# Performance work log

Hardware: AMD Instinct MI355X
Metric: run time of the kernel (lower is better)

## Reference

```python
import jax, jax.numpy as jnp
import numpy as np

E = 32      # particle_embed_dim = q/k/v head out dim
G = 2       # nof_net_types (conv groups)
NEG_SLOPE = 0.01


def _glin(x, w, b, groups):
    """Grouped 1x1 conv on (M, C, 1, 1) == grouped linear.
    x: (M, Cin), w: (Cout, Cin//groups), b: (Cout,)."""
    M = x.shape[0]
    Cout = w.shape[0]
    xg = x.reshape(M, groups, -1)                 # (M, G, Cin/G)
    wg = w.reshape(groups, Cout // groups, -1)    # (G, Cout/G, Cin/G)
    y = jnp.einsum('mgi,goi->mgo', xg, wg).reshape(M, Cout)
    return y + b


def setup_inputs() -> dict:
    key = jax.random.key(0)
    ks = jax.random.split(key, 9)
    B, N = 32, 1024
    s = 0.05
    return {
        'x_e':   jax.random.normal(ks[0], (B, N, G * E), dtype=jnp.float32),
        'w_qkv': jax.random.normal(ks[1], (3 * G * E, E), dtype=jnp.float32) * s,
        'b_qkv': jax.random.normal(ks[2], (3 * G * E,), dtype=jnp.float32) * s,
        'w_h1':  jax.random.normal(ks[3], (G * E, 2 * E), dtype=jnp.float32) * s,
        'b_h1':  jax.random.normal(ks[4], (G * E,), dtype=jnp.float32) * s,
        'w_h10': jax.random.normal(ks[5], (G * E, E), dtype=jnp.float32) * s,
        'b_h10': jax.random.normal(ks[6], (G * E,), dtype=jnp.float32) * s,
        'w_h11': jax.random.normal(ks[7], (G * E, E), dtype=jnp.float32) * s,
        'b_h11': jax.random.normal(ks[8], (G * E,), dtype=jnp.float32) * s,
    }


def reference(x_e, w_qkv, b_qkv, w_h1, b_h1, w_h10, b_h10, w_h11, b_h11):
    B, N, D = x_e.shape                      # D = G*E = 64
    act = lambda z: jnp.where(z >= 0, z, NEG_SLOPE * z)

    # grouped 1x1-conv QKV projection
    qkv = _glin(x_e.reshape(B * N, D), w_qkv, b_qkv, G)        # (B*N, 3*G*E)
    qkv = qkv.reshape(B, N, G, 3, E).transpose(0, 2, 3, 1, 4)  # (B, G, 3, N, E)
    q, k, v = qkv[:, :, 0], qkv[:, :, 1], qkv[:, :, 2]         # each (B, G, N, E)

    # NOTE: module divides k by sqrt(E) and logits by sqrt(E) again -> 1/E total
    scale = 1.0 / E
    ip = jnp.einsum('bgne,bgme->bgnm', q, k) * scale           # (B, G, N, N)
    sip = jax.nn.softmax(ip, axis=-1)
    attn = jnp.einsum('bgnm,bgme->bgne', sip, v)               # (B, G, N, E)

    # concat pre-attention v with attention output, regroup per-particle
    x_xe = jnp.concatenate([v, attn], axis=3)                  # (B, G, N, 2E)
    x_xe = x_xe.transpose(0, 2, 1, 3).reshape(B * N, G * 2 * E)  # (B*N, 128)

    h = act(_glin(x_xe, w_h1, b_h1, G))
    h = act(_glin(h, w_h10, b_h10, G))
    h = act(_glin(h, w_h11, b_h11, G))
    return h.reshape(B * N, G * E, 1, 1)
```

## Files before the change

### kernel.cpp

```cpp
#include <hip/hip_runtime.h>

#define B_ 32
#define N_ 1024
#define NEG 0.01f
#define QSC (1.4426950408889634f/32.0f)

using half8  = __attribute__((ext_vector_type(8))) _Float16;
using half4  = __attribute__((ext_vector_type(4))) _Float16;
using half2  = __attribute__((ext_vector_type(2))) _Float16;
using fp16x2 = __attribute__((ext_vector_type(2))) __fp16;
using floatx4 = __attribute__((ext_vector_type(4))) float;

#if defined(__has_builtin)
#if __has_builtin(__builtin_amdgcn_exp2f)
#define EXP2(x) __builtin_amdgcn_exp2f(x)
#endif
#endif
#ifndef EXP2
#define EXP2(x) exp2f(x)
#endif

__device__ inline half2 pkcvt(float a, float b) {
    fp16x2 r = __builtin_amdgcn_cvt_pkrtz(a, b);
    return __builtin_bit_cast(half2, r);
}

__device__ inline half8 cvt8(float4 a, float4 b) {
    half2 p0 = pkcvt(a.x, a.y);
    half2 p1 = pkcvt(a.z, a.w);
    half2 p2 = pkcvt(b.x, b.y);
    half2 p3 = pkcvt(b.z, b.w);
    half8 h = { p0[0],p0[1], p1[0],p1[1], p2[0],p2[1], p3[0],p3[1] };
    return h;
}

struct __align__(16) Smem {
    _Float16 wsh[96*36];
    float    bsh[96];
    _Float16 Kst[2][128*40];
    _Float16 Vtst[2][32*136];
    union {
        _Float16 qs[128*40];
        _Float16 xs[128*72];
    } u;
    float linv[128];
    float bl1[32], bl10[32], bl11[32];
};

__global__ __launch_bounds__(256, 2) void fused_kernel(
    const float* __restrict__ x, const float* __restrict__ w_qkv, const float* __restrict__ b_qkv,
    const float* __restrict__ w_h1,  const float* __restrict__ b_h1,
    const float* __restrict__ w_h10, const float* __restrict__ b_h10,
    const float* __restrict__ w_h11, const float* __restrict__ b_h11,
    float* __restrict__ out)
{
    __shared__ Smem sm;
    int t = threadIdx.x;
    int bg = blockIdx.x >> 3;
    int qtile = blockIdx.x & 7;
    int b = bg >> 1, g = bg & 1;
    int qbase = qtile * 128;
    int lane = t & 63, w = t >> 6;
    int L15 = lane & 15, quad = lane >> 4;

    for (int idx = t; idx < 96*32; idx += 256) {
        int r = idx >> 5, c = idx & 31;
        float wv = w_qkv[(g*96 + r)*32 + c];
        sm.wsh[r*36 + c] = (_Float16)(r < 32 ? wv*QSC : wv);
    }
    if (t < 96) sm.bsh[t] = b_qkv[g*96 + t];
    if (t < 32) {
        sm.bl1[t]  = b_h1[g*32+t];
        sm.bl10[t] = b_h10[g*32+t];
        sm.bl11[t] = b_h11[g*32+t];
    }
    __syncthreads();

    half8 bwq[2], bwk[2], bwv[2];
    floatx4 cq[2], ck[2], cv[2];
    #pragma unroll
    for (int et = 0; et < 2; et++) {
        bwq[et] = *(const half8*)&sm.wsh[(     et*16 + L15)*36 + quad*8];
        bwk[et] = *(const half8*)&sm.wsh[(32 + et*16 + L15)*36 + quad*8];
        bwv[et] = *(const half8*)&sm.wsh[(64 + et*16 + L15)*36 + quad*8];
        float bq = sm.bsh[     et*16 + L15] * QSC;
        float bk = sm.bsh[32 + et*16 + L15];
        float bv = sm.bsh[64 + et*16 + L15];
        cq[et] = (floatx4){bq,bq,bq,bq};
        ck[et] = (floatx4){bk,bk,bk,bk};
        cv[et] = (floatx4){bv,bv,bv,bv};
    }

    {
        floatx4 dq[2][2];
        #pragma unroll
        for (int mt = 0; mt < 2; mt++) {
            const float* p = x + ((size_t)b*N_ + qbase + w*32 + mt*16 + L15)*64 + g*32 + quad*8;
            half8 axq = cvt8(*(const float4*)p, *(const float4*)(p + 4));
            dq[mt][0] = __builtin_amdgcn_mfma_f32_16x16x32_f16(axq, bwq[0], cq[0], 0,0,0);
            dq[mt][1] = __builtin_amdgcn_mfma_f32_16x16x32_f16(axq, bwq[1], cq[1], 0,0,0);
        }
        #pragma unroll
        for (int mt = 0; mt < 2; mt++)
            #pragma unroll
            for (int et = 0; et < 2; et++)
                #pragma unroll
                for (int r = 0; r < 4; r++)
                    sm.u.qs[(w*32 + mt*16 + quad*4 + r)*40 + et*16 + L15] =
                        (_Float16)dq[mt][et][r];
    }
    __syncthreads();
    half8 bq0 = *(const half8*)&sm.u.qs[(w*32 +      L15)*40 + quad*8];
    half8 bq1 = *(const half8*)&sm.u.qs[(w*32 + 16 + L15)*40 + quad*8];

    float4 xf0[2], xf1[2];
    auto prefetch = [&](int tile) {
        #pragma unroll
        for (int mt = 0; mt < 2; mt++) {
            const float* p = x + ((size_t)b*N_ + tile*128 + w*32 + mt*16 + L15)*64 + g*32 + quad*8;
            xf0[mt] = *(const float4*)p;
            xf1[mt] = *(const float4*)(p + 4);
        }
    };
    auto proj_tile = [&](int tile, int buf) {
        floatx4 dK[2][2], dV[2][2];
        #pragma unroll
        for (int mt = 0; mt < 2; mt++) {
            half8 axk = cvt8(xf0[mt], xf1[mt]);
            dK[mt][0] = __builtin_amdgcn_mfma_f32_16x16x32_f16(axk, bwk[0], ck[0], 0,0,0);
            dK[mt][1] = __builtin_amdgcn_mfma_f32_16x16x32_f16(axk, bwk[1], ck[1], 0,0,0);
            dV[mt][0] = __builtin_amdgcn_mfma_f32_16x16x32_f16(axk, bwv[0], cv[0], 0,0,0);
            dV[mt][1] = __builtin_amdgcn_mfma_f32_16x16x32_f16(axk, bwv[1], cv[1], 0,0,0);
        }
        #pragma unroll
        for (int mt = 0; mt < 2; mt++) {
            int rb = w*32 + mt*16 + quad*4;
            #pragma unroll
            for (int et = 0; et < 2; et++) {
                half2 k01 = pkcvt(dK[mt][et][0], dK[mt][et][1]);
                half2 k23 = pkcvt(dK[mt][et][2], dK[mt][et][3]);
                half2 v01 = pkcvt(dV[mt][et][0], dV[mt][et][1]);
                half2 v23 = pkcvt(dV[mt][et][2], dV[mt][et][3]);
                half4 vh = { v01[0], v01[1], v23[0], v23[1] };
                sm.Kst[buf][(rb+0)*40 + et*16 + L15] = k01[0];
                sm.Kst[buf][(rb+1)*40 + et*16 + L15] = k01[1];
                sm.Kst[buf][(rb+2)*40 + et*16 + L15] = k23[0];
                sm.Kst[buf][(rb+3)*40 + et*16 + L15] = k23[1];
                *(half4*)&sm.Vtst[buf][(et*16 + L15)*136 + rb] = vh;
                if (tile == qtile) {
                    #pragma unroll
                    for (int r = 0; r < 4; r++)
                        sm.u.xs[(rb + r)*72 + et*16 + L15] = vh[r];
                }
            }
        }
    };

    prefetch(0);
    proj_tile(0, 0);
    __syncthreads();

    floatx4 o00 = {0.f,0.f,0.f,0.f}, o01 = o00, o10 = o00, o11 = o00;
    float lsum0 = 0.f, lsum1 = 0.f;

    for (int kt = 0; kt < 8; kt++) {
        int cur = kt & 1;
        if (kt < 7) prefetch(kt + 1);
        #pragma unroll
        for (int mt8 = 0; mt8 < 8; mt8++) {
            half8 ak = *(const half8*)&sm.Kst[cur][(mt8*16 + L15)*40 + quad*8];
            floatx4 zz = {0.f,0.f,0.f,0.f};
            floatx4 s0 = __builtin_amdgcn_mfma_f32_16x16x32_f16(ak, bq0, zz, 0,0,0);
            floatx4 s1 = __builtin_amdgcn_mfma_f32_16x16x32_f16(ak, bq1, zz, 0,0,0);
            float p00 = EXP2(s0.x), p01 = EXP2(s0.y), p02 = EXP2(s0.z), p03 = EXP2(s0.w);
            float p10 = EXP2(s1.x), p11 = EXP2(s1.y), p12 = EXP2(s1.z), p13 = EXP2(s1.w);
            lsum0 += (p00+p01)+(p02+p03);
            lsum1 += (p10+p11)+(p12+p13);
            half2 pa = pkcvt(p00, p01);
            half2 pb = pkcvt(p02, p03);
            half2 pc = pkcvt(p10, p11);
            half2 pd = pkcvt(p12, p13);
            half4 a0 = { pa[0], pa[1], pb[0], pb[1] };
            half4 a1 = { pc[0], pc[1], pd[0], pd[1] };
            half4 bv0 = *(const half4*)&sm.Vtst[cur][      L15*136 + mt8*16 + quad*4];
            half4 bv1 = *(const half4*)&sm.Vtst[cur][(16 + L15)*136 + mt8*16 + quad*4];
            o00 = __builtin_amdgcn_mfma_f32_16x16x16f16(a0, bv0, o00, 0,0,0);
            o01 = __builtin_amdgcn_mfma_f32_16x16x16f16(a0, bv1, o01, 0,0,0);
            o10 = __builtin_amdgcn_mfma_f32_16x16x16f16(a1, bv0, o10, 0,0,0);
            o11 = __builtin_amdgcn_mfma_f32_16x16x16f16(a1, bv1, o11, 0,0,0);
        }
        if (kt < 7) proj_tile(kt + 1, 1 - cur);
        __syncthreads();
    }

    lsum0 += __shfl_xor(lsum0, 16, 64); lsum0 += __shfl_xor(lsum0, 32, 64);
    lsum1 += __shfl_xor(lsum1, 16, 64); lsum1 += __shfl_xor(lsum1, 32, 64);
    if (quad == 0) {
        sm.linv[w*32 +      L15] = 1.0f / lsum0;
        sm.linv[w*32 + 16 + L15] = 1.0f / lsum1;
    }
    __syncthreads();

    {
        const floatx4* ofr[2][2] = { {&o00,&o01}, {&o10,&o11} };
        #pragma unroll
        for (int nt = 0; nt < 2; nt++) {
            float4 li = *(const float4*)&sm.linv[w*32 + nt*16 + quad*4];
            #pragma unroll
            for (int et = 0; et < 2; et++) {
                floatx4 ov = *ofr[nt][et];
                sm.u.xs[(w*32+nt*16+quad*4+0)*72 + 32 + et*16 + L15] = (_Float16)(ov[0]*li.x);
                sm.u.xs[(w*32+nt*16+quad*4+1)*72 + 32 + et*16 + L15] = (_Float16)(ov[1]*li.y);
                sm.u.xs[(w*32+nt*16+quad*4+2)*72 + 32 + et*16 + L15] = (_Float16)(ov[2]*li.z);
                sm.u.xs[(w*32+nt*16+quad*4+3)*72 + 32 + et*16 + L15] = (_Float16)(ov[3]*li.w);
            }
        }
    }
    __syncthreads();

    half4 a1f[2][4], a2f[2][2], a3f[2][2];
    #pragma unroll
    for (int mt = 0; mt < 2; mt++) {
        #pragma unroll
        for (int kt = 0; kt < 4; kt++) {
            float4 f = *(const float4*)(w_h1 + (size_t)(g*32+mt*16+L15)*64 + kt*16 + quad*4);
            half2 ha = pkcvt(f.x, f.y);
            half2 hb = pkcvt(f.z, f.w);
            half4 h = { ha[0], ha[1], hb[0], hb[1] };
            a1f[mt][kt] = h;
        }
        #pragma unroll
        for (int kt = 0; kt < 2; kt++) {
            float4 f = *(const float4*)(w_h10 + (size_t)(g*32+mt*16+L15)*32 + kt*16 + quad*4);
            half2 ha = pkcvt(f.x, f.y);
            half2 hb = pkcvt(f.z, f.w);
            half4 h = { ha[0], ha[1], hb[0], hb[1] };
            a2f[mt][kt] = h;
            float4 f2 = *(const float4*)(w_h11 + (size_t)(g*32+mt*16+L15)*32 + kt*16 + quad*4);
            half2 hc = pkcvt(f2.x, f2.y);
            half2 hd = pkcvt(f2.z, f2.w);
            half4 h2 = { hc[0], hc[1], hd[0], hd[1] };
            a3f[mt][kt] = h2;
        }
    }

    floatx4 d1[2][2];
    #pragma unroll
    for (int mt = 0; mt < 2; mt++) {
        float4 bb = *(const float4*)&sm.bl1[mt*16 + quad*4];
        floatx4 seed = { bb.x, bb.y, bb.z, bb.w };
        d1[mt][0] = seed; d1[mt][1] = seed;
    }
    #pragma unroll
    for (int nt = 0; nt < 2; nt++)
        #pragma unroll
        for (int kt = 0; kt < 4; kt++) {
            half4 b1 = *(const half4*)&sm.u.xs[(w*32+nt*16+L15)*72 + kt*16 + quad*4];
            d1[0][nt] = __builtin_amdgcn_mfma_f32_16x16x16f16(a1f[0][kt], b1, d1[0][nt], 0,0,0);
            d1[1][nt] = __builtin_amdgcn_mfma_f32_16x16x16f16(a1f[1][kt], b1, d1[1][nt], 0,0,0);
        }
    half4 h1b[2][2];
    #pragma unroll
    for (int mt = 0; mt < 2; mt++)
        #pragma unroll
        for (int nt = 0; nt < 2; nt++) {
            float v0 = d1[mt][nt][0]; v0 = (v0>=0.f)?v0:NEG*v0;
            float v1 = d1[mt][nt][1]; v1 = (v1>=0.f)?v1:NEG*v1;
            float v2 = d1[mt][nt][2]; v2 = (v2>=0.f)?v2:NEG*v2;
            float v3 = d1[mt][nt][3]; v3 = (v3>=0.f)?v3:NEG*v3;
            half2 ha = pkcvt(v0, v1);
            half2 hb = pkcvt(v2, v3);
            half4 h = { ha[0], ha[1], hb[0], hb[1] };
            h1b[mt][nt] = h;
        }
    floatx4 d2[2][2];
    #pragma unroll
    for (int mt = 0; mt < 2; mt++) {
        float4 bb = *(const float4*)&sm.bl10[mt*16 + quad*4];
        floatx4 seed = { bb.x, bb.y, bb.z, bb.w };
        d2[mt][0] = seed; d2[mt][1] = seed;
    }
    #pragma unroll
    for (int mt = 0; mt < 2; mt++)
        #pragma unroll
        for (int nt = 0; nt < 2; nt++)
            #pragma unroll
            for (int kt = 0; kt < 2; kt++)
                d2[mt][nt] = __builtin_amdgcn_mfma_f32_16x16x16f16(a2f[mt][kt], h1b[kt][nt], d2[mt][nt], 0,0,0);
    half4 h2b[2][2];
    #pragma unroll
    for (int mt = 0; mt < 2; mt++)
        #pragma unroll
        for (int nt = 0; nt < 2; nt++) {
            float v0 = d2[mt][nt][0]; v0 = (v0>=0.f)?v0:NEG*v0;
            float v1 = d2[mt][nt][1]; v1 = (v1>=0.f)?v1:NEG*v1;
            float v2 = d2[mt][nt][2]; v2 = (v2>=0.f)?v2:NEG*v2;
            float v3 = d2[mt][nt][3]; v3 = (v3>=0.f)?v3:NEG*v3;
            half2 ha = pkcvt(v0, v1);
            half2 hb = pkcvt(v2, v3);
            half4 h = { ha[0], ha[1], hb[0], hb[1] };
            h2b[mt][nt] = h;
        }
    floatx4 d3[2][2];
    #pragma unroll
    for (int mt = 0; mt < 2; mt++) {
        float4 bb = *(const float4*)&sm.bl11[mt*16 + quad*4];
        floatx4 seed = { bb.x, bb.y, bb.z, bb.w };
        d3[mt][0] = seed; d3[mt][1] = seed;
    }
    #pragma unroll
    for (int mt = 0; mt < 2; mt++)
        #pragma unroll
        for (int nt = 0; nt < 2; nt++)
            #pragma unroll
            for (int kt = 0; kt < 2; kt++)
                d3[mt][nt] = __builtin_amdgcn_mfma_f32_16x16x16f16(a3f[mt][kt], h2b[kt][nt], d3[mt][nt], 0,0,0);
    #pragma unroll
    for (int mt = 0; mt < 2; mt++)
        #pragma unroll
        for (int nt = 0; nt < 2; nt++) {
            float4 ov;
            ov.x = d3[mt][nt][0]; ov.x = (ov.x>=0.f)?ov.x:NEG*ov.x;
            ov.y = d3[mt][nt][1]; ov.y = (ov.y>=0.f)?ov.y:NEG*ov.y;
            ov.z = d3[mt][nt][2]; ov.z = (ov.z>=0.f)?ov.z:NEG*ov.z;
            ov.w = d3[mt][nt][3]; ov.w = (ov.w>=0.f)?ov.w:NEG*ov.w;
            *(float4*)(out + ((size_t)b*N_ + qbase + w*32 + nt*16 + L15)*64 + g*32 + mt*16 + quad*4) = ov;
        }
}

extern "C" void kernel_launch(void* const* d_in, const int* in_sizes, int n_in,
                              void* d_out, int out_size, void* d_ws, size_t ws_size,
                              hipStream_t stream) {
    const float* x_e   = (const float*)d_in[0];
    const float* w_qkv = (const float*)d_in[1];
    const float* b_qkv = (const float*)d_in[2];
    const float* w_h1  = (const float*)d_in[3];
    const float* b_h1  = (const float*)d_in[4];
    const float* w_h10 = (const float*)d_in[5];
    const float* b_h10 = (const float*)d_in[6];
    const float* w_h11 = (const float*)d_in[7];
    const float* b_h11 = (const float*)d_in[8];
    float* out = (float*)d_out;

    hipLaunchKernelGGL(fused_kernel, dim3(B_*2*8), dim3(256), 0, stream,
                       x_e, w_qkv, b_qkv, w_h1, b_h1, w_h10, b_h10, w_h11, b_h11, out);
}
```

Measured before the change: 98.32 us.

## Split QKV projection into separate kernel and stream fp16 K/V via LDS DMA

The single fused kernel, which recomputed the K/V projection for every key tile in every query block, becomes two kernels. A projection kernel writes Q, K, V and transposed V in fp16 to workspace once. The attention kernel then streams K/V tiles straight into LDS with global_load_lds double buffering and uses a swizzled V layout. It runs smaller 64-query blocks with two waves splitting the key range, merging partial sums through LDS, raises occupancy to 4 blocks per SM and remaps block indices. This removes the redundant projection work, at the cost of an extra launch and a global-memory round trip through the workspace.

```diff
diff --git a/kernel.cpp b/kernel.cpp
--- a/kernel.cpp
+++ b/kernel.cpp
@@ -20,6 +20,9 @@
 #define EXP2(x) exp2f(x)
 #endif
 
+#define MFMA32 __builtin_amdgcn_mfma_f32_16x16x32_f16
+#define MFMA16 __builtin_amdgcn_mfma_f32_16x16x16f16
+
 __device__ inline half2 pkcvt(float a, float b) {
     fp16x2 r = __builtin_amdgcn_cvt_pkrtz(a, b);
     return __builtin_bit_cast(half2, r);
@@ -34,32 +37,33 @@
     return h;
 }
 
-struct __align__(16) Smem {
-    _Float16 wsh[96*36];
-    float    bsh[96];
-    _Float16 Kst[2][128*40];
-    _Float16 Vtst[2][32*136];
-    union {
-        _Float16 qs[128*40];
-        _Float16 xs[128*72];
-    } u;
-    float linv[128];
-    float bl1[32], bl10[32], bl11[32];
-};
-
-__global__ __launch_bounds__(256, 2) void fused_kernel(
+__device__ __forceinline__ void gload16(const _Float16* g, _Float16* l) {
+#if defined(__has_builtin) && __has_builtin(__builtin_amdgcn_global_load_lds)
+    __builtin_amdgcn_global_load_lds(
+        (const __attribute__((address_space(1))) unsigned int*)g,
+        (__attribute__((address_space(3))) unsigned int*)l, 16, 0, 0);
+#else
+    int lane = threadIdx.x & 63;
+    *(half8*)(l + lane*8) = *(const half8*)g;
+#endif
+}
+
+__global__ __launch_bounds__(256, 2) void proj_kernel(
     const float* __restrict__ x, const float* __restrict__ w_qkv, const float* __restrict__ b_qkv,
-    const float* __restrict__ w_h1,  const float* __restrict__ b_h1,
-    const float* __restrict__ w_h10, const float* __restrict__ b_h10,
-    const float* __restrict__ w_h11, const float* __restrict__ b_h11,
-    float* __restrict__ out)
+    _Float16* __restrict__ Qs, _Float16* __restrict__ Kg,
+    _Float16* __restrict__ Vg, _Float16* __restrict__ Vtg)
 {
-    __shared__ Smem sm;
+    __shared__ struct __align__(16) {
+        _Float16 wsh[96*36];
+        float    bsh[96];
+        _Float16 qk[128*72];
+        _Float16 vrow[128*32];
+        _Float16 vt[32*136];
+    } sm;
     int t = threadIdx.x;
     int bg = blockIdx.x >> 3;
-    int qtile = blockIdx.x & 7;
+    int qt = blockIdx.x & 7;
     int b = bg >> 1, g = bg & 1;
-    int qbase = qtile * 128;
     int lane = t & 63, w = t >> 6;
     int L15 = lane & 15, quad = lane >> 4;
 
@@ -69,11 +73,6 @@
         sm.wsh[r*36 + c] = (_Float16)(r < 32 ? wv*QSC : wv);
     }
     if (t < 96) sm.bsh[t] = b_qkv[g*96 + t];
-    if (t < 32) {
-        sm.bl1[t]  = b_h1[g*32+t];
-        sm.bl10[t] = b_h10[g*32+t];
-        sm.bl11[t] = b_h11[g*32+t];
-    }
     __syncthreads();
 
     half8 bwq[2], bwk[2], bwv[2];
@@ -91,87 +90,126 @@
         cv[et] = (floatx4){bv,bv,bv,bv};
     }
 
+    #pragma unroll
+    for (int mt = 0; mt < 2; mt++) {
+        const float* p = x + ((size_t)b*N_ + qt*128 + w*32 + mt*16 + L15)*64 + g*32 + quad*8;
+        half8 ax = cvt8(*(const float4*)p, *(const float4*)(p + 4));
+        floatx4 dQ[2], dK[2], dV[2];
+        #pragma unroll
+        for (int et = 0; et < 2; et++) {
+            dQ[et] = MFMA32(ax, bwq[et], cq[et], 0,0,0);
+            dK[et] = MFMA32(ax, bwk[et], ck[et], 0,0,0);
+            dV[et] = MFMA32(ax, bwv[et], cv[et], 0,0,0);
+        }
+        int rb = w*32 + mt*16 + quad*4;
+        #pragma unroll
+        for (int et = 0; et < 2; et++) {
+            #pragma unroll
+            for (int r = 0; r < 4; r++)
+                sm.qk[(rb+r)*72 + et*16 + L15] = (_Float16)dQ[et][r];
+            half2 k01 = pkcvt(dK[et][0], dK[et][1]);
+            half2 k23 = pkcvt(dK[et][2], dK[et][3]);
+            sm.qk[(rb+0)*72 + 32 + et*16 + L15] = k01[0];
+            sm.qk[(rb+1)*72 + 32 + et*16 + L15] = k01[1];
+            sm.qk[(rb+2)*72 + 32 + et*16 + L15] = k23[0];
+            sm.qk[(rb+3)*72 + 32 + et*16 + L15] = k23[1];
+            half2 v01 = pkcvt(dV[et][0], dV[et][1]);
+            half2 v23 = pkcvt(dV[et][2], dV[et][3]);
+            half4 vh = { v01[0], v01[1], v23[0], v23[1] };
+            sm.vrow[(rb+0)*32 + et*16 + L15] = vh[0];
+            sm.vrow[(rb+1)*32 + et*16 + L15] = vh[1];
+            sm.vrow[(rb+2)*32 + et*16 + L15] = vh[2];
+            sm.vrow[(rb+3)*32 + et*16 + L15] = vh[3];
+            *(half4*)&sm.vt[(et*16 + L15)*136 + rb] = vh;
+        }
+    }
+    __syncthreads();
+
     {
-        floatx4 dq[2][2];
-        #pragma unroll
-        for (int mt = 0; mt < 2; mt++) {
-            const float* p = x + ((size_t)b*N_ + qbase + w*32 + mt*16 + L15)*64 + g*32 + quad*8;
-            half8 axq = cvt8(*(const float4*)p, *(const float4*)(p + 4));
-            dq[mt][0] = __builtin_amdgcn_mfma_f32_16x16x32_f16(axq, bwq[0], cq[0], 0,0,0);
-            dq[mt][1] = __builtin_amdgcn_mfma_f32_16x16x32_f16(axq, bwq[1], cq[1], 0,0,0);
-        }
-        #pragma unroll
-        for (int mt = 0; mt < 2; mt++)
-            #pragma unroll
-            for (int et = 0; et < 2; et++)
-                #pragma unroll
-                for (int r = 0; r < 4; r++)
-                    sm.u.qs[(w*32 + mt*16 + quad*4 + r)*40 + et*16 + L15] =
-                        (_Float16)dq[mt][et][r];
-    }
-    __syncthreads();
-    half8 bq0 = *(const half8*)&sm.u.qs[(w*32 +      L15)*40 + quad*8];
-    half8 bq1 = *(const half8*)&sm.u.qs[(w*32 + 16 + L15)*40 + quad*8];
-
-    float4 xf0[2], xf1[2];
-    auto prefetch = [&](int tile) {
-        #pragma unroll
-        for (int mt = 0; mt < 2; mt++) {
-            const float* p = x + ((size_t)b*N_ + tile*128 + w*32 + mt*16 + L15)*64 + g*32 + quad*8;
-            xf0[mt] = *(const float4*)p;
-            xf1[mt] = *(const float4*)(p + 4);
+        int row = t >> 1, sel = t & 1;
+        const float4* s4 = (const float4*)&sm.qk[row*72 + sel*32];
+        float4* d4 = (float4*)((sel ? Kg : Qs) + ((size_t)bg*1024 + qt*128 + row)*32);
+        d4[0]=s4[0]; d4[1]=s4[1]; d4[2]=s4[2]; d4[3]=s4[3];
+    }
+    if (t < 128) {
+        const float4* s4 = (const float4*)&sm.vrow[t*32];
+        float4* d4 = (float4*)(Vg + ((size_t)bg*1024 + qt*128 + t)*32);
+        d4[0]=s4[0]; d4[1]=s4[1]; d4[2]=s4[2]; d4[3]=s4[3];
+    }
+    {
+        int e = t >> 3, c = t & 7;
+        const float4* s4 = (const float4*)&sm.vt[e*136 + c*16];
+        float4* d4 = (float4*)(Vtg + ((size_t)bg*32 + e)*1024 + qt*128 + c*16);
+        d4[0]=s4[0]; d4[1]=s4[1];
+    }
+}
+
+__global__ __launch_bounds__(256, 4) void attn_kernel(
+    const _Float16* __restrict__ Qs, const _Float16* __restrict__ Kg,
+    const _Float16* __restrict__ Vg, const _Float16* __restrict__ Vtg,
+    const float* __restrict__ w_h1,  const float* __restrict__ b_h1,
+    const float* __restrict__ w_h10, const float* __restrict__ b_h10,
+    const float* __restrict__ w_h11, const float* __restrict__ b_h11,
+    float* __restrict__ out)
+{
+    __shared__ struct __align__(16) {
+        _Float16 Kt[2][2][64*32];
+        _Float16 Vt[2][2][32*64];
+        _Float16 xs[64*40];
+        float    linv[64];
+    } sm;
+    int t = threadIdx.x;
+    int bid = blockIdx.x;
+    int map = (bid & 7)*128 + (bid >> 3);
+    int bg = map >> 4, qt = map & 15;
+    int b = bg >> 1, g = bg & 1;
+    int lane = t & 63, w = t >> 6;
+    int L15 = lane & 15, quad = lane >> 4;
+    int qg = w >> 1, h = w & 1;
+    int qbase = qt*64;
+    int lr = qg*32;
+    int l7s = (L15 & 7) << 3;
+
+    const _Float16* qrow = Qs + ((size_t)bg*1024 + qbase + lr)*32;
+    half8 bq0 = *(const half8*)(qrow + (size_t)L15*32 + quad*8);
+    half8 bq1 = *(const half8*)(qrow + (size_t)(16 + L15)*32 + quad*8);
+
+    const _Float16* kg0 = Kg + (size_t)bg*32768 + lane*8;
+    int er = lane >> 3;
+    int vswz = ((lane & 7)*8) ^ (er << 3);
+    const _Float16* vg0 = Vtg + (size_t)bg*32768 + (size_t)er*1024 + vswz;
+
+    auto stage = [&](int tile, int buf) {
+        _Float16* kl = &sm.Kt[buf][h][0];
+        _Float16* vl = &sm.Vt[buf][h][0];
+        const _Float16* kgt = kg0 + (size_t)tile*2048;
+        const _Float16* vgt = vg0 + (size_t)tile*64;
+        #pragma unroll
+        for (int c = 0; c < 2; c++) {
+            int cc = qg*2 + c;
+            gload16(kgt + cc*512,          kl + cc*512);
+            gload16(vgt + (size_t)cc*8192, vl + cc*512);
         }
     };
-    auto proj_tile = [&](int tile, int buf) {
-        floatx4 dK[2][2], dV[2][2];
-        #pragma unroll
-        for (int mt = 0; mt < 2; mt++) {
-            half8 axk = cvt8(xf0[mt], xf1[mt]);
-            dK[mt][0] = __builtin_amdgcn_mfma_f32_16x16x32_f16(axk, bwk[0], ck[0], 0,0,0);
-            dK[mt][1] = __builtin_amdgcn_mfma_f32_16x16x32_f16(axk, bwk[1], ck[1], 0,0,0);
-            dV[mt][0] = __builtin_amdgcn_mfma_f32_16x16x32_f16(axk, bwv[0], cv[0], 0,0,0);
-            dV[mt][1] = __builtin_amdgcn_mfma_f32_16x16x32_f16(axk, bwv[1], cv[1], 0,0,0);
-        }
-        #pragma unroll
-        for (int mt = 0; mt < 2; mt++) {
-            int rb = w*32 + mt*16 + quad*4;
-            #pragma unroll
-            for (int et = 0; et < 2; et++) {
-                half2 k01 = pkcvt(dK[mt][et][0], dK[mt][et][1]);
-                half2 k23 = pkcvt(dK[mt][et][2], dK[mt][et][3]);
-                half2 v01 = pkcvt(dV[mt][et][0], dV[mt][et][1]);
-                half2 v23 = pkcvt(dV[mt][et][2], dV[mt][et][3]);
-                half4 vh = { v01[0], v01[1], v23[0], v23[1] };
-                sm.Kst[buf][(rb+0)*40 + et*16 + L15] = k01[0];
-                sm.Kst[buf][(rb+1)*40 + et*16 + L15] = k01[1];
-                sm.Kst[buf][(rb+2)*40 + et*16 + L15] = k23[0];
-                sm.Kst[buf][(rb+3)*40 + et*16 + L15] = k23[1];
-                *(half4*)&sm.Vtst[buf][(et*16 + L15)*136 + rb] = vh;
-                if (tile == qtile) {
-                    #pragma unroll
-                    for (int r = 0; r < 4; r++)
-                        sm.u.xs[(rb + r)*72 + et*16 + L15] = vh[r];
-                }
-            }
-        }
-    };
-
-    prefetch(0);
-    proj_tile(0, 0);
-    __syncthreads();
-
-    floatx4 o00 = {0.f,0.f,0.f,0.f}, o01 = o00, o10 = o00, o11 = o00;
+
+    const floatx4 zz = {0.f,0.f,0.f,0.f};
+    floatx4 o00 = zz, o01 = zz, o10 = zz, o11 = zz;
     float lsum0 = 0.f, lsum1 = 0.f;
 
-    for (int kt = 0; kt < 8; kt++) {
-        int cur = kt & 1;
-        if (kt < 7) prefetch(kt + 1);
-        #pragma unroll
-        for (int mt8 = 0; mt8 < 8; mt8++) {
-            half8 ak = *(const half8*)&sm.Kst[cur][(mt8*16 + L15)*40 + quad*8];
-            floatx4 zz = {0.f,0.f,0.f,0.f};
-            floatx4 s0 = __builtin_amdgcn_mfma_f32_16x16x32_f16(ak, bq0, zz, 0,0,0);
-            floatx4 s1 = __builtin_amdgcn_mfma_f32_16x16x32_f16(ak, bq1, zz, 0,0,0);
+    int buf = 0;
+    stage(h*8, 0);
+    __syncthreads();
+
+    for (int i = 0; i < 8; i++) {
+        if (i < 7) stage(h*8 + i + 1, buf ^ 1);
+        const _Float16* Kl = &sm.Kt[buf][h][0];
+        const _Float16* Vl = &sm.Vt[buf][h][0];
+        __builtin_amdgcn_s_setprio(1);
+        #pragma unroll
+        for (int m8 = 0; m8 < 4; m8++) {
+            half8 ak = *(const half8*)&Kl[(m8*16 + L15)*32 + quad*8];
+            floatx4 s0 = MFMA32(ak, bq0, zz, 0,0,0);
+            floatx4 s1 = MFMA32(ak, bq1, zz, 0,0,0);
             float p00 = EXP2(s0.x), p01 = EXP2(s0.y), p02 = EXP2(s0.z), p03 = EXP2(s0.w);
             float p10 = EXP2(s1.x), p11 = EXP2(s1.y), p12 = EXP2(s1.z), p13 = EXP2(s1.w);
             lsum0 += (p00+p01)+(p02+p03);
@@ -182,42 +220,63 @@
             half2 pd = pkcvt(p12, p13);
             half4 a0 = { pa[0], pa[1], pb[0], pb[1] };
             half4 a1 = { pc[0], pc[1], pd[0], pd[1] };
-            half4 bv0 = *(const half4*)&sm.Vtst[cur][      L15*136 + mt8*16 + quad*4];
-            half4 bv1 = *(const half4*)&sm.Vtst[cur][(16 + L15)*136 + mt8*16 + quad*4];
-            o00 = __builtin_amdgcn_mfma_f32_16x16x16f16(a0, bv0, o00, 0,0,0);
-            o01 = __builtin_amdgcn_mfma_f32_16x16x16f16(a0, bv1, o01, 0,0,0);
-            o10 = __builtin_amdgcn_mfma_f32_16x16x16f16(a1, bv0, o10, 0,0,0);
-            o11 = __builtin_amdgcn_mfma_f32_16x16x16f16(a1, bv1, o11, 0,0,0);
-        }
-        if (kt < 7) proj_tile(kt + 1, 1 - cur);
+            int vi = (m8*16 + quad*4) ^ l7s;
+            half4 bv0 = *(const half4*)&Vl[L15*64 + vi];
+            half4 bv1 = *(const half4*)&Vl[(16 + L15)*64 + vi];
+            o00 = MFMA16(a0, bv0, o00, 0,0,0);
+            o01 = MFMA16(a0, bv1, o01, 0,0,0);
+            o10 = MFMA16(a1, bv0, o10, 0,0,0);
+            o11 = MFMA16(a1, bv1, o11, 0,0,0);
+        }
+        __builtin_amdgcn_s_setprio(0);
         __syncthreads();
+        buf ^= 1;
     }
 
     lsum0 += __shfl_xor(lsum0, 16, 64); lsum0 += __shfl_xor(lsum0, 32, 64);
     lsum1 += __shfl_xor(lsum1, 16, 64); lsum1 += __shfl_xor(lsum1, 32, 64);
-    if (quad == 0) {
-        sm.linv[w*32 +      L15] = 1.0f / lsum0;
-        sm.linv[w*32 + 16 + L15] = 1.0f / lsum1;
-    }
-    __syncthreads();
-
-    {
+
+    float* obuf  = (float*)&sm.Kt[0][0][0];
+    float* lpart = (float*)&sm.Vt[0][0][0];
+    if (h == 1) {
+        float4* ob = (float4*)&obuf[((size_t)qg*64 + lane)*16];
+        ob[0] = (float4){o00[0],o00[1],o00[2],o00[3]};
+        ob[1] = (float4){o01[0],o01[1],o01[2],o01[3]};
+        ob[2] = (float4){o10[0],o10[1],o10[2],o10[3]};
+        ob[3] = (float4){o11[0],o11[1],o11[2],o11[3]};
+        if (quad == 0) { lpart[qg*32 + L15] = lsum0; lpart[qg*32 + 16 + L15] = lsum1; }
+    }
+    __syncthreads();
+    if (h == 0) {
+        const float4* ob = (const float4*)&obuf[((size_t)qg*64 + lane)*16];
+        float4 t0 = ob[0], t1 = ob[1], t2 = ob[2], t3 = ob[3];
+        o00[0]+=t0.x; o00[1]+=t0.y; o00[2]+=t0.z; o00[3]+=t0.w;
+        o01[0]+=t1.x; o01[1]+=t1.y; o01[2]+=t1.z; o01[3]+=t1.w;
+        o10[0]+=t2.x; o10[1]+=t2.y; o10[2]+=t2.z; o10[3]+=t2.w;
+        o11[0]+=t3.x; o11[1]+=t3.y; o11[2]+=t3.z; o11[3]+=t3.w;
+        float li0 = 1.0f/(lsum0 + lpart[qg*32 + L15]);
+        float li1 = 1.0f/(lsum1 + lpart[qg*32 + 16 + L15]);
+        if (quad == 0) { sm.linv[qg*32 + L15] = li0; sm.linv[qg*32 + 16 + L15] = li1; }
+    }
+    __syncthreads();
+    if (h == 0) {
         const floatx4* ofr[2][2] = { {&o00,&o01}, {&o10,&o11} };
         #pragma unroll
         for (int nt = 0; nt < 2; nt++) {
-            float4 li = *(const float4*)&sm.linv[w*32 + nt*16 + quad*4];
+            float4 li = *(const float4*)&sm.linv[qg*32 + nt*16 + quad*4];
             #pragma unroll
             for (int et = 0; et < 2; et++) {
                 floatx4 ov = *ofr[nt][et];
-                sm.u.xs[(w*32+nt*16+quad*4+0)*72 + 32 + et*16 + L15] = (_Float16)(ov[0]*li.x);
-                sm.u.xs[(w*32+nt*16+quad*4+1)*72 + 32 + et*16 + L15] = (_Float16)(ov[1]*li.y);
-                sm.u.xs[(w*32+nt*16+quad*4+2)*72 + 32 + et*16 + L15] = (_Float16)(ov[2]*li.z);
-                sm.u.xs[(w*32+nt*16+quad*4+3)*72 + 32 + et*16 + L15] = (_Float16)(ov[3]*li.w);
+                sm.xs[(qg*32+nt*16+quad*4+0)*40 + et*16 + L15] = (_Float16)(ov[0]*li.x);
+                sm.xs[(qg*32+nt*16+quad*4+1)*40 + et*16 + L15] = (_Float16)(ov[1]*li.y);
+                sm.xs[(qg*32+nt*16+quad*4+2)*40 + et*16 + L15] = (_Float16)(ov[2]*li.z);
+                sm.xs[(qg*32+nt*16+quad*4+3)*40 + et*16 + L15] = (_Float16)(ov[3]*li.w);
             }
         }
     }
     __syncthreads();
 
+    int lrh = qg*32 + h*16;
     half4 a1f[2][4], a2f[2][2], a3f[2][2];
     #pragma unroll
     for (int mt = 0; mt < 2; mt++) {
@@ -226,16 +285,16 @@
             float4 f = *(const float4*)(w_h1 + (size_t)(g*32+mt*16+L15)*64 + kt*16 + quad*4);
             half2 ha = pkcvt(f.x, f.y);
             half2 hb = pkcvt(f.z, f.w);
-            half4 h = { ha[0], ha[1], hb[0], hb[1] };
-            a1f[mt][kt] = h;
+            half4 hh = { ha[0], ha[1], hb[0], hb[1] };
+            a1f[mt][kt] = hh;
         }
         #pragma unroll
         for (int kt = 0; kt < 2; kt++) {
             float4 f = *(const float4*)(w_h10 + (size_t)(g*32+mt*16+L15)*32 + kt*16 + quad*4);
             half2 ha = pkcvt(f.x, f.y);
             half2 hb = pkcvt(f.z, f.w);
-            half4 h = { ha[0], ha[1], hb[0], hb[1] };
-            a2f[mt][kt] = h;
+            half4 hh = { ha[0], ha[1], hb[0], hb[1] };
+            a2f[mt][kt] = hh;
             float4 f2 = *(const float4*)(w_h11 + (size_t)(g*32+mt*16+L15)*32 + kt*16 + quad*4);
             half2 hc = pkcvt(f2.x, f2.y);
             half2 hd = pkcvt(f2.z, f2.w);
@@ -244,88 +303,72 @@
         }
     }
 
-    floatx4 d1[2][2];
-    #pragma unroll
-    for (int mt = 0; mt < 2; mt++) {
-        float4 bb = *(const float4*)&sm.bl1[mt*16 + quad*4];
-        floatx4 seed = { bb.x, bb.y, bb.z, bb.w };
-        d1[mt][0] = seed; d1[mt][1] = seed;
-    }
-    #pragma unroll
-    for (int nt = 0; nt < 2; nt++)
-        #pragma unroll
-        for (int kt = 0; kt < 4; kt++) {
-            half4 b1 = *(const half4*)&sm.u.xs[(w*32+nt*16+L15)*72 + kt*16 + quad*4];
-            d1[0][nt] = __builtin_amdgcn_mfma_f32_16x16x16f16(a1f[0][kt], b1, d1[0][nt], 0,0,0);
-            d1[1][nt] = __builtin_amdgcn_mfma_f32_16x16x16f16(a1f[1][kt], b1, d1[1][nt], 0,0,0);
-        }
-    half4 h1b[2][2];
-    #pragma unroll
-    for (int mt = 0; mt < 2; mt++)
-        #pragma unroll
-        for (int nt = 0; nt < 2; nt++) {
-            float v0 = d1[mt][nt][0]; v0 = (v0>=0.f)?v0:NEG*v0;
-            float v1 = d1[mt][nt][1]; v1 = (v1>=0.f)?v1:NEG*v1;
-            float v2 = d1[mt][nt][2]; v2 = (v2>=0.f)?v2:NEG*v2;
-            float v3 = d1[mt][nt][3]; v3 = (v3>=0.f)?v3:NEG*v3;
-            half2 ha = pkcvt(v0, v1);
-            half2 hb = pkcvt(v2, v3);
-            half4 h = { ha[0], ha[1], hb[0], hb[1] };
-            h1b[mt][nt] = h;
-        }
-    floatx4 d2[2][2];
-    #pragma unroll
-    for (int mt = 0; mt < 2; mt++) {
-        float4 bb = *(const float4*)&sm.bl10[mt*16 + quad*4];
-        floatx4 seed = { bb.x, bb.y, bb.z, bb.w };
-        d2[mt][0] = seed; d2[mt][1] = seed;
-    }
-    #pragma unroll
-    for (int mt = 0; mt < 2; mt++)
-        #pragma unroll
-        for (int nt = 0; nt < 2; nt++)
-            #pragma unroll
-            for (int kt = 0; kt < 2; kt++)
-                d2[mt][nt] = __builtin_amdgcn_mfma_f32_16x16x16f16(a2f[mt][kt], h1b[kt][nt], d2[mt][nt], 0,0,0);
-    half4 h2b[2][2];
-    #pragma unroll
-    for (int mt = 0; mt < 2; mt++)
-        #pragma unroll
-        for (int nt = 0; nt < 2; nt++) {
-            float v0 = d2[mt][nt][0]; v0 = (v0>=0.f)?v0:NEG*v0;
-            float v1 = d2[mt][nt][1]; v1 = (v1>=0.f)?v1:NEG*v1;
-            float v2 = d2[mt][nt][2]; v2 = (v2>=0.f)?v2:NEG*v2;
-            float v3 = d2[mt][nt][3]; v3 = (v3>=0.f)?v3:NEG*v3;
-            half2 ha = pkcvt(v0, v1);
-            half2 hb = pkcvt(v2, v3);
-            half4 h = { ha[0], ha[1], hb[0], hb[1] };
-            h2b[mt][nt] = h;
-        }
-    floatx4 d3[2][2];
-    #pragma unroll
-    for (int mt = 0; mt < 2; mt++) {
-        float4 bb = *(const float4*)&sm.bl11[mt*16 + quad*4];
-        floatx4 seed = { bb.x, bb.y, bb.z, bb.w };
-        d3[mt][0] = seed; d3[mt][1] = seed;
-    }
-    #pragma unroll
-    for (int mt = 0; mt < 2; mt++)
-        #pragma unroll
-        for (int nt = 0; nt < 2; nt++)
-            #pragma unroll
-            for (int kt = 0; kt < 2; kt++)
-                d3[mt][nt] = __builtin_amdgcn_mfma_f32_16x16x16f16(a3f[mt][kt], h2b[kt][nt], d3[mt][nt], 0,0,0);
-    #pragma unroll
-    for (int mt = 0; mt < 2; mt++)
-        #pragma unroll
-        for (int nt = 0; nt < 2; nt++) {
-            float4 ov;
-            ov.x = d3[mt][nt][0]; ov.x = (ov.x>=0.f)?ov.x:NEG*ov.x;
-            ov.y = d3[mt][nt][1]; ov.y = (ov.y>=0.f)?ov.y:NEG*ov.y;
-            ov.z = d3[mt][nt][2]; ov.z = (ov.z>=0.f)?ov.z:NEG*ov.z;
-            ov.w = d3[mt][nt][3]; ov.w = (ov.w>=0.f)?ov.w:NEG*ov.w;
-            *(float4*)(out + ((size_t)b*N_ + qbase + w*32 + nt*16 + L15)*64 + g*32 + mt*16 + quad*4) = ov;
-        }
+    floatx4 d1[2];
+    #pragma unroll
+    for (int mt = 0; mt < 2; mt++) {
+        float4 bb = *(const float4*)(b_h1 + g*32 + mt*16 + quad*4);
+        d1[mt] = (floatx4){bb.x, bb.y, bb.z, bb.w};
+    }
+    size_t grow = (size_t)bg*1024 + qbase + lrh + L15;
+    #pragma unroll
+    for (int kt = 0; kt < 4; kt++) {
+        half4 b1;
+        if (kt < 2) b1 = *(const half4*)(Vg + grow*32 + kt*16 + quad*4);
+        else        b1 = *(const half4*)&sm.xs[(lrh + L15)*40 + (kt-2)*16 + quad*4];
+        d1[0] = MFMA16(a1f[0][kt], b1, d1[0], 0,0,0);
+        d1[1] = MFMA16(a1f[1][kt], b1, d1[1], 0,0,0);
+    }
+    half4 h1b[2];
+    #pragma unroll
+    for (int mt = 0; mt < 2; mt++) {
+        float v0 = d1[mt][0]; v0 = (v0>=0.f)?v0:NEG*v0;
+        float v1 = d1[mt][1]; v1 = (v1>=0.f)?v1:NEG*v1;
+        float v2 = d1[mt][2]; v2 = (v2>=0.f)?v2:NEG*v2;
+        float v3 = d1[mt][3]; v3 = (v3>=0.f)?v3:NEG*v3;
+        half2 ha = pkcvt(v0, v1);
+        half2 hb = pkcvt(v2, v3);
+        half4 hh = { ha[0], ha[1], hb[0], hb[1] };
+        h1b[mt] = hh;
+    }
+    floatx4 d2[2];
+    #pragma unroll
+    for (int mt = 0; mt < 2; mt++) {
+        float4 bb = *(const float4*)(b_h10 + g*32 + mt*16 + quad*4);
+        d2[mt] = (floatx4){bb.x, bb.y, bb.z, bb.w};
+        #pragma unroll
+        for (int kt = 0; kt < 2; kt++)
+            d2[mt] = MFMA16(a2f[mt][kt], h1b[kt], d2[mt], 0,0,0);
+    }
+    half4 h2b[2];
+    #pragma unroll
+    for (int mt = 0; mt < 2; mt++) {
+        float v0 = d2[mt][0]; v0 = (v0>=0.f)?v0:NEG*v0;
+        float v1 = d2[mt][1]; v1 = (v1>=0.f)?v1:NEG*v1;
+        float v2 = d2[mt][2]; v2 = (v2>=0.f)?v2:NEG*v2;
+        float v3 = d2[mt][3]; v3 = (v3>=0.f)?v3:NEG*v3;
+        half2 ha = pkcvt(v0, v1);
+        half2 hb = pkcvt(v2, v3);
+        half4 hh = { ha[0], ha[1], hb[0], hb[1] };
+        h2b[mt] = hh;
+    }
+    floatx4 d3[2];
+    #pragma unroll
+    for (int mt = 0; mt < 2; mt++) {
+        float4 bb = *(const float4*)(b_h11 + g*32 + mt*16 + quad*4);
+        d3[mt] = (floatx4){bb.x, bb.y, bb.z, bb.w};
+        #pragma unroll
+        for (int kt = 0; kt < 2; kt++)
+            d3[mt] = MFMA16(a3f[mt][kt], h2b[kt], d3[mt], 0,0,0);
+    }
+    #pragma unroll
+    for (int mt = 0; mt < 2; mt++) {
+        float4 ov;
+        ov.x = d3[mt][0]; ov.x = (ov.x>=0.f)?ov.x:NEG*ov.x;
+        ov.y = d3[mt][1]; ov.y = (ov.y>=0.f)?ov.y:NEG*ov.y;
+        ov.z = d3[mt][2]; ov.z = (ov.z>=0.f)?ov.z:NEG*ov.z;
+        ov.w = d3[mt][3]; ov.w = (ov.w>=0.f)?ov.w:NEG*ov.w;
+        *(float4*)(out + ((size_t)b*N_ + qbase + lrh + L15)*64 + g*32 + mt*16 + quad*4) = ov;
+    }
 }
 
 extern "C" void kernel_launch(void* const* d_in, const int* in_sizes, int n_in,
@@ -342,6 +385,14 @@
     const float* b_h11 = (const float*)d_in[8];
     float* out = (float*)d_out;
 
-    hipLaunchKernelGGL(fused_kernel, dim3(B_*2*8), dim3(256), 0, stream,
-                       x_e, w_qkv, b_qkv, w_h1, b_h1, w_h10, b_h10, w_h11, b_h11, out);
-}
+    _Float16* base = (_Float16*)d_ws;
+    _Float16* Qs  = base;
+    _Float16* Kg  = base + (1u<<21);
+    _Float16* Vg  = base + (2u<<21);
+    _Float16* Vtg = base + (3u<<21);
+
+    hipLaunchKernelGGL(proj_kernel, dim3(512), dim3(256), 0, stream,
+                       x_e, w_qkv, b_qkv, Qs, Kg, Vg, Vtg);
+    hipLaunchKernelGGL(attn_kernel, dim3(1024), dim3(256), 0, stream,
+                       Qs, Kg, Vg, Vtg, w_h1, b_h1, w_h10, b_h10, w_h11, b_h11, out);
+}
```

Measured after the change: 110.3 us. +12.1%, slower.
